# Optimization experiments

Hardware: AMD Instinct MI355X
Metric: run time of the kernel (lower is better)

Reference implementation:

```python
import math
import jax, jax.numpy as jnp
import numpy as np


def setup_inputs() -> dict:
    key = jax.random.key(0)
    kq, kk, kv = jax.random.split(key, 3)
    bs, n_tok, n_heads, width = 2, 2048, 8, 64
    deg = 32  # neighbors per dst token -> coo_cnt_max
    q = jax.random.normal(kq, (bs, n_tok, n_heads, width), dtype=jnp.float32)
    k = jax.random.normal(kk, (bs, n_tok, n_heads, width), dtype=jnp.float32)
    v = jax.random.normal(kv, (bs, n_tok, n_heads, width), dtype=jnp.float32)
    rng = np.random.default_rng(0)
    dst = np.repeat(np.arange(n_tok), deg)            # [cl]
    src = rng.integers(0, n_tok, size=n_tok * deg)    # [cl]
    sm = np.tile(np.arange(deg), n_tok)               # [cl], unique per dst
    coo = jnp.asarray(np.stack([dst, src, sm], axis=1), dtype=jnp.int32)  # [cl,3]
    return {"q": q, "k": k, "v": v, "coo": coo, "coo_cnt_max": deg}


def reference(q, k, v, coo, coo_cnt_max):
    bs, n_tok, n_heads, width = q.shape
    dst, src, sm = coo[:, 0], coo[:, 1], coo[:, 2]
    # [b, h, t, w] layout
    qq = q.transpose(0, 2, 1, 3)
    kk = k.transpose(0, 2, 1, 3)
    vv = v.transpose(0, 2, 1, 3)
    scale = -1.0 / math.sqrt(width)
    # per-edge negative scaled L1 distance: [b, h, cl]
    ww = jnp.sum(jnp.abs(qq[:, :, dst, :] - kk[:, :, src, :]), axis=-1) * scale
    neg_big = jnp.asarray(-1e32, dtype=q.dtype)
    # scatter edge scores into dense padded attention slots: [b, h, t, cnt+1]
    attn = jnp.full((bs, n_heads, n_tok, coo_cnt_max + 1), neg_big, dtype=q.dtype)
    attn = attn.at[:, :, dst, sm].set(ww)
    attn_sm = jax.nn.softmax(attn, axis=-1)
    # scatter values into padded neighbor-value tensor: [b, h, t, cnt+1, w]
    vw = jnp.zeros((bs, n_heads, n_tok, coo_cnt_max + 1, width), dtype=q.dtype)
    vw = vw.at[:, :, dst, sm, :].set(vv[:, :, src, :])
    vo = jnp.einsum('bhds,bhdsw->bdhw', attn_sm, vw)
    # only dst tokens appearing in coo receive output; others stay zero
    vout = jnp.zeros_like(v).at[:, dst, :, :].set(vo[:, dst, :, :])
    return vout
```

## Files before the change

### kernel.cpp

```cpp
#include <hip/hip_runtime.h>
#include <hip/hip_bf16.h>

#define BS   2
#define NT   2048
#define NH   8
#define WD   64
#define DEG  32

#define PK_ROWS   (BS * 4 * NT)
#define PK_ROW_B  512
#define PK_UINTS  (PK_ROWS * (PK_ROW_B / 4))

typedef _Float16 half2_t __attribute__((ext_vector_type(2)));

#if defined(__has_builtin)
#if __has_builtin(__builtin_amdgcn_fdot2)
#define HAVE_FDOT2 1
#endif
#endif

__device__ __forceinline__ unsigned short f2h(float f) {
    _Float16 h = (_Float16)f;
    unsigned short u; __builtin_memcpy(&u, &h, 2); return u;
}
__device__ __forceinline__ half2_t u2h2(unsigned int w) {
    half2_t r; __builtin_memcpy(&r, &w, 4); return r;
}
__device__ __forceinline__ half2_t habs2(half2_t x) {
    unsigned int u; __builtin_memcpy(&u, &x, 4);
    u &= 0x7fff7fffu;
    half2_t r; __builtin_memcpy(&r, &u, 4); return r;
}

__global__ __launch_bounds__(256) void pack_kv_f16(
    const float* __restrict__ k,
    const float* __restrict__ v,
    unsigned int* __restrict__ packed)
{
    const int u    = blockIdx.x * 256 + threadIdx.x;
    const int row  = u >> 7;
    const int pos  = u & 127;
    const int part = pos >> 6;
    const int e    = pos & 63;
    const int s    = row & (NT - 1);
    const int hp   = (row >> 11) & 3;
    const int b    = row >> 13;
    const int elem = e * 2;
    const int h_in = elem >> 6;
    const int w0   = elem & 63;

    const float* src = (part == 0 ? k : v)
        + (((size_t)(b * NT + s) * NH + hp * 2 + h_in) << 6) + w0;
    float2 f = *(const float2*)src;
    packed[u] = (unsigned int)f2h(f.x) | ((unsigned int)f2h(f.y) << 16);
}

__global__ __launch_bounds__(64) void l1attn_main_f16(
    const float* __restrict__ q,
    const unsigned int* __restrict__ packed,
    const int* __restrict__ coo,
    float* __restrict__ out)
{
    const int bid   = blockIdx.x;
    const int combo = bid & 7;
    const int hp    = combo & 3;
    const int b     = combo >> 2;
    const int t     = bid >> 3;
    const int ln    = threadIdx.x;
    const int hw    = ln >> 5;
    const int l     = ln & 31;

    __shared__ int          s_src[DEG];
    __shared__ unsigned int s_q[64];
    __shared__ unsigned int s_k[DEG * 128];

    if (ln < DEG) {
        s_src[ln] = coo[(t * DEG + ln) * 3 + 1];
    }
    {
        const float2* qrow = (const float2*)
            (q + ((size_t)(b * NT + t) * NH + hp * 2) * WD);
        float2 qv = qrow[ln];
        s_q[ln] = (unsigned int)f2h(qv.x) | ((unsigned int)f2h(qv.y) << 16);
    }
    __syncthreads();

    {
        #pragma unroll
        for (int r = 0; r < 16; ++r) {
            const int j = 2 * r + hw;
            const int s = s_src[j];
            const int chunk = (l + j) & 31;
            const char* gaddr = (const char*)packed
                + ((size_t)((b * 4 + hp) * NT + s)) * PK_ROW_B + chunk * 16;
            char* laddr = (char*)s_k + 2 * r * PK_ROW_B;
            __builtin_amdgcn_global_load_lds(
                (const __attribute__((address_space(1))) void*)gaddr,
                (__attribute__((address_space(3))) void*)laddr,
                16, 0, 0);
        }
    }
    __syncthreads();

    float acc = 0.f;
#ifdef HAVE_FDOT2
    const half2_t one2 = {(_Float16)1.0f, (_Float16)1.0f};
#endif
    #pragma unroll
    for (int i = 0; i < 8; ++i) {
        const int slot = ((hw * 8 + i) - l) & 31;
        uint4 c = *(const uint4*)((const char*)s_k + l * PK_ROW_B + slot * 16);
        const unsigned int ws[4] = {c.x, c.y, c.z, c.w};
        #pragma unroll
        for (int m = 0; m < 4; ++m) {
            half2_t kh = u2h2(ws[m]);
            half2_t qh = u2h2(s_q[hw * 32 + i * 4 + m]);
            half2_t ad = habs2(qh - kh);
#ifdef HAVE_FDOT2
            acc = __builtin_amdgcn_fdot2(ad, one2, acc, false);
#else
            acc += (float)ad.x + (float)ad.y;
#endif
        }
    }
    float logit = -0.125f * acc;

    float m = logit;
    #pragma unroll
    for (int d = 16; d >= 1; d >>= 1) m = fmaxf(m, __shfl_xor(m, d));
    float e = __expf(logit - m);
    float ssum = e;
    #pragma unroll
    for (int d = 16; d >= 1; d >>= 1) ssum += __shfl_xor(ssum, d);
    const float p = e / ssum;

    int p2i;
    {
        _Float16 ph = (_Float16)p;
        half2_t p2 = {ph, ph};
        __builtin_memcpy(&p2i, &p2, 4);
    }
    const int gv   = 16 + hw * 8 + (l >> 2);
    const int boff = (l & 3) * 4;
    half2_t acc2 = {(_Float16)0.0f, (_Float16)0.0f};
    #pragma unroll 8
    for (int j = 0; j < DEG; ++j) {
        const int pj2i = __shfl(p2i, j, 32);
        const int slot = (gv - j) & 31;
        unsigned int w = *(const unsigned int*)
            ((const char*)s_k + j * PK_ROW_B + slot * 16 + boff);
        acc2 = __builtin_elementwise_fma(u2h2(pj2i), u2h2(w), acc2);
    }

    const int h = hp * 2 + hw;
    float2 res = make_float2((float)acc2.x, (float)acc2.y);
    *(float2*)(out + ((size_t)(b * NT + t) * NH + h) * WD + 2 * l) = res;
}

__global__ __launch_bounds__(64) void l1attn_sparse_fp32(
    const float* __restrict__ q,
    const float* __restrict__ k,
    const float* __restrict__ v,
    const int* __restrict__ coo,
    float* __restrict__ out)
{
    const int bid   = blockIdx.x;
    const int combo = bid & 7;
    const int hp    = combo & 3;
    const int b     = combo >> 2;
    const int t     = bid >> 3;
    const int ln    = threadIdx.x;
    const int hw    = ln >> 5;
    const int l     = ln & 31;

    __shared__ int   s_src[DEG];
    __shared__ float s_q[2 * WD];
    __shared__ float s_k[DEG * 2 * WD];

    if (ln < DEG) s_src[ln] = coo[(t * DEG + ln) * 3 + 1];
    {
        const float2* qrow = (const float2*)
            (q + ((size_t)(b * NT + t) * NH + hp * 2) * WD);
        float2 qv = qrow[ln];
        s_q[2 * ln] = qv.x; s_q[2 * ln + 1] = qv.y;
    }
    __syncthreads();
    {
        #pragma unroll
        for (int r = 0; r < 16; ++r) {
            const int j = 2 * r + hw;
            const int s = s_src[j];
            const int chunk = (l + j) & 31;
            const float* gaddr = k + ((size_t)(b * NT + s) * NH + hp * 2) * WD
                               + chunk * 4;
            float* laddr = s_k + 2 * r * (2 * WD);
            __builtin_amdgcn_global_load_lds(
                (const __attribute__((address_space(1))) void*)gaddr,
                (__attribute__((address_space(3))) void*)laddr, 16, 0, 0);
        }
    }
    const int h  = hp * 2 + hw;
    const int jg = l >> 4;
    const int wq = l & 15;
    float4 vr[16];
    #pragma unroll
    for (int i = 0; i < 16; ++i) {
        const int sv = s_src[2 * i + jg];
        vr[i] = *(const float4*)(v + ((size_t)(b * NT + sv) * NH + h) * WD + 4 * wq);
    }
    __syncthreads();
    const float* qh = s_q + hw * WD;
    float acc = 0.f;
    #pragma unroll
    for (int i = 0; i < 16; ++i) {
        const int slot = ((hw * 16 + i) - l) & 31;
        float4 kv = *(const float4*)(s_k + l * (2 * WD) + slot * 4);
        const int wb = i * 4;
        acc += fabsf(qh[wb] - kv.x) + fabsf(qh[wb + 1] - kv.y)
             + fabsf(qh[wb + 2] - kv.z) + fabsf(qh[wb + 3] - kv.w);
    }
    float logit = -0.125f * acc;
    float m = logit;
    #pragma unroll
    for (int d = 16; d >= 1; d >>= 1) m = fmaxf(m, __shfl_xor(m, d));
    float e = __expf(logit - m);
    float ssum = e;
    #pragma unroll
    for (int d = 16; d >= 1; d >>= 1) ssum += __shfl_xor(ssum, d);
    const float p = e / ssum;
    float4 o4 = make_float4(0.f, 0.f, 0.f, 0.f);
    #pragma unroll
    for (int i = 0; i < 16; ++i) {
        const float pj = __shfl(p, 2 * i + jg, 32);
        o4.x += pj * vr[i].x; o4.y += pj * vr[i].y;
        o4.z += pj * vr[i].z; o4.w += pj * vr[i].w;
    }
    o4.x += __shfl_xor(o4.x, 16); o4.y += __shfl_xor(o4.y, 16);
    o4.z += __shfl_xor(o4.z, 16); o4.w += __shfl_xor(o4.w, 16);
    if (jg == 0)
        *(float4*)(out + ((size_t)(b * NT + t) * NH + h) * WD + 4 * wq) = o4;
}

extern "C" void kernel_launch(void* const* d_in, const int* in_sizes, int n_in,
                              void* d_out, int out_size, void* d_ws, size_t ws_size,
                              hipStream_t stream) {
    const float* q   = (const float*)d_in[0];
    const float* k   = (const float*)d_in[1];
    const float* v   = (const float*)d_in[2];
    const int*   coo = (const int*)d_in[3];
    float*       o   = (float*)d_out;

    if (ws_size >= (size_t)PK_UINTS * 4) {
        unsigned int* packed = (unsigned int*)d_ws;
        hipLaunchKernelGGL(pack_kv_f16, dim3(PK_UINTS / 256), dim3(256), 0,
                           stream, k, v, packed);
        hipLaunchKernelGGL(l1attn_main_f16, dim3(BS * NT * 4), dim3(64), 0,
                           stream, q, packed, coo, o);
    } else {
        hipLaunchKernelGGL(l1attn_sparse_fp32, dim3(BS * NT * 4), dim3(64), 0,
                           stream, q, k, v, coo, o);
    }
}
```

Measured before the change: 108.8 us.

## Process several tokens per block with double-buffered async LDS prefetch

Each 64-thread block now handles 8 destination tokens instead of one, so the grid shrinks by 8x. The coo source indices and the q rows for all 8 tokens are loaded up front. The gathered K/V rows for the next token are prefetched into a second LDS buffer with global_load_lds while the current token is computed. Manual vmcnt waits replace the block barriers. This is meant to hide gather latency and amortise per-block setup, but it cuts the number of resident waves and doubles LDS per block, which may reduce latency hiding across the GPU.

Measured after the change: 114.7 us. 1.05x slower.

```diff
diff --git a/kernel.cpp b/kernel.cpp
--- a/kernel.cpp
+++ b/kernel.cpp
@@ -6,6 +6,7 @@
 #define NH   8
 #define WD   64
 #define DEG  32
+#define TPB  8
 
 #define PK_ROWS   (BS * 4 * NT)
 #define PK_ROW_B  512
@@ -65,96 +66,114 @@
     const int combo = bid & 7;
     const int hp    = combo & 3;
     const int b     = combo >> 2;
-    const int t     = bid >> 3;
+    const int tbase = (bid >> 3) * TPB;
     const int ln    = threadIdx.x;
     const int hw    = ln >> 5;
     const int l     = ln & 31;
 
-    __shared__ int          s_src[DEG];
-    __shared__ unsigned int s_q[64];
-    __shared__ unsigned int s_k[DEG * 128];
-
-    if (ln < DEG) {
-        s_src[ln] = coo[(t * DEG + ln) * 3 + 1];
-    }
-    {
+    __shared__ int          s_src[TPB * DEG];
+    __shared__ unsigned int s_q[TPB * 64];
+    __shared__ unsigned int s_buf[2][DEG * 128];
+
+    #pragma unroll
+    for (int x = 0; x < (TPB * DEG) / 64; ++x) {
+        const int idx = x * 64 + ln;
+        const int tt  = idx >> 5, j = idx & 31;
+        s_src[idx] = coo[((tbase + tt) * DEG + j) * 3 + 1];
+    }
+    #pragma unroll
+    for (int tt = 0; tt < TPB; ++tt) {
         const float2* qrow = (const float2*)
-            (q + ((size_t)(b * NT + t) * NH + hp * 2) * WD);
+            (q + ((size_t)(b * NT + tbase + tt) * NH + hp * 2) * WD);
         float2 qv = qrow[ln];
-        s_q[ln] = (unsigned int)f2h(qv.x) | ((unsigned int)f2h(qv.y) << 16);
-    }
-    __syncthreads();
-
-    {
+        s_q[tt * 64 + ln] = (unsigned int)f2h(qv.x)
+                          | ((unsigned int)f2h(qv.y) << 16);
+    }
+    asm volatile("s_waitcnt vmcnt(0)" ::: "memory");
+
+    auto issue = [&](int pb, int tt) {
         #pragma unroll
         for (int r = 0; r < 16; ++r) {
             const int j = 2 * r + hw;
-            const int s = s_src[j];
+            const int s = s_src[tt * DEG + j];
             const int chunk = (l + j) & 31;
             const char* gaddr = (const char*)packed
                 + ((size_t)((b * 4 + hp) * NT + s)) * PK_ROW_B + chunk * 16;
-            char* laddr = (char*)s_k + 2 * r * PK_ROW_B;
+            char* laddr = (char*)&s_buf[pb][0] + 2 * r * PK_ROW_B;
             __builtin_amdgcn_global_load_lds(
                 (const __attribute__((address_space(1))) void*)gaddr,
                 (__attribute__((address_space(3))) void*)laddr,
                 16, 0, 0);
         }
-    }
-    __syncthreads();
-
-    float acc = 0.f;
+    };
+
+    issue(0, 0);
+
+    #pragma unroll
+    for (int it = 0; it < TPB; ++it) {
+        if (it + 1 < TPB) issue((it + 1) & 1, it + 1);
+
+        if (it == 0)            asm volatile("s_waitcnt vmcnt(16)" ::: "memory");
+        else if (it == TPB - 1) asm volatile("s_waitcnt vmcnt(1)"  ::: "memory");
+        else                    asm volatile("s_waitcnt vmcnt(17)" ::: "memory");
+
+        const unsigned int* buf = &s_buf[it & 1][0];
+
+        float acc = 0.f;
 #ifdef HAVE_FDOT2
-    const half2_t one2 = {(_Float16)1.0f, (_Float16)1.0f};
-#endif
-    #pragma unroll
-    for (int i = 0; i < 8; ++i) {
-        const int slot = ((hw * 8 + i) - l) & 31;
-        uint4 c = *(const uint4*)((const char*)s_k + l * PK_ROW_B + slot * 16);
-        const unsigned int ws[4] = {c.x, c.y, c.z, c.w};
-        #pragma unroll
-        for (int m = 0; m < 4; ++m) {
-            half2_t kh = u2h2(ws[m]);
-            half2_t qh = u2h2(s_q[hw * 32 + i * 4 + m]);
-            half2_t ad = habs2(qh - kh);
+        const half2_t one2 = {(_Float16)1.0f, (_Float16)1.0f};
+#endif
+        #pragma unroll
+        for (int i = 0; i < 8; ++i) {
+            const int slot = ((hw * 8 + i) - l) & 31;
+            uint4 c = *(const uint4*)((const char*)buf + l * PK_ROW_B + slot * 16);
+            const unsigned int ws[4] = {c.x, c.y, c.z, c.w};
+            #pragma unroll
+            for (int m = 0; m < 4; ++m) {
+                half2_t kh = u2h2(ws[m]);
+                half2_t qh = u2h2(s_q[it * 64 + hw * 32 + i * 4 + m]);
+                half2_t ad = habs2(qh - kh);
 #ifdef HAVE_FDOT2
-            acc = __builtin_amdgcn_fdot2(ad, one2, acc, false);
+                acc = __builtin_amdgcn_fdot2(ad, one2, acc, false);
 #else
-            acc += (float)ad.x + (float)ad.y;
-#endif
-        }
-    }
-    float logit = -0.125f * acc;
-
-    float m = logit;
-    #pragma unroll
-    for (int d = 16; d >= 1; d >>= 1) m = fmaxf(m, __shfl_xor(m, d));
-    float e = __expf(logit - m);
-    float ssum = e;
-    #pragma unroll
-    for (int d = 16; d >= 1; d >>= 1) ssum += __shfl_xor(ssum, d);
-    const float p = e / ssum;
-
-    int p2i;
-    {
-        _Float16 ph = (_Float16)p;
-        half2_t p2 = {ph, ph};
-        __builtin_memcpy(&p2i, &p2, 4);
-    }
-    const int gv   = 16 + hw * 8 + (l >> 2);
-    const int boff = (l & 3) * 4;
-    half2_t acc2 = {(_Float16)0.0f, (_Float16)0.0f};
-    #pragma unroll 8
-    for (int j = 0; j < DEG; ++j) {
-        const int pj2i = __shfl(p2i, j, 32);
-        const int slot = (gv - j) & 31;
-        unsigned int w = *(const unsigned int*)
-            ((const char*)s_k + j * PK_ROW_B + slot * 16 + boff);
-        acc2 = __builtin_elementwise_fma(u2h2(pj2i), u2h2(w), acc2);
-    }
-
-    const int h = hp * 2 + hw;
-    float2 res = make_float2((float)acc2.x, (float)acc2.y);
-    *(float2*)(out + ((size_t)(b * NT + t) * NH + h) * WD + 2 * l) = res;
+                acc += (float)ad.x + (float)ad.y;
+#endif
+            }
+        }
+        float logit = -0.125f * acc;
+
+        float m = logit;
+        #pragma unroll
+        for (int d = 16; d >= 1; d >>= 1) m = fmaxf(m, __shfl_xor(m, d));
+        float e = __expf(logit - m);
+        float ssum = e;
+        #pragma unroll
+        for (int d = 16; d >= 1; d >>= 1) ssum += __shfl_xor(ssum, d);
+        const float p = e / ssum;
+
+        int p2i;
+        {
+            _Float16 ph = (_Float16)p;
+            half2_t p2 = {ph, ph};
+            __builtin_memcpy(&p2i, &p2, 4);
+        }
+        const int gv   = 16 + hw * 8 + (l >> 2);
+        const int boff = (l & 3) * 4;
+        half2_t acc2 = {(_Float16)0.0f, (_Float16)0.0f};
+        #pragma unroll 8
+        for (int j = 0; j < DEG; ++j) {
+            const int pj2i = __shfl(p2i, j, 32);
+            const int slot = (gv - j) & 31;
+            unsigned int w = *(const unsigned int*)
+                ((const char*)buf + j * PK_ROW_B + slot * 16 + boff);
+            acc2 = __builtin_elementwise_fma(u2h2(pj2i), u2h2(w), acc2);
+        }
+
+        const int h = hp * 2 + hw;
+        const int t = tbase + it;
+        float2 res = make_float2((float)acc2.x, (float)acc2.y);
+        *(float2*)(out + ((size_t)(b * NT + t) * NH + h) * WD + 2 * l) = res;
+    }
 }
 
 __global__ __launch_bounds__(64) void l1attn_sparse_fp32(
@@ -254,8 +273,8 @@
         unsigned int* packed = (unsigned int*)d_ws;
         hipLaunchKernelGGL(pack_kv_f16, dim3(PK_UINTS / 256), dim3(256), 0,
                            stream, k, v, packed);
-        hipLaunchKernelGGL(l1attn_main_f16, dim3(BS * NT * 4), dim3(64), 0,
-                           stream, q, packed, coo, o);
+        hipLaunchKernelGGL(l1attn_main_f16, dim3((BS * NT * 4) / TPB), dim3(64),
+                           0, stream, q, packed, coo, o);
     } else {
         hipLaunchKernelGGL(l1attn_sparse_fp32, dim3(BS * NT * 4), dim3(64), 0,
                            stream, q, k, v, coo, o);
```

## Stage only K to LDS and load V into registers, overlapping with L1 compute

Applied to the files above, without the earlier changes.

The f16 main kernel now copies only the K half of each packed neighbor row into LDS, which halves shared memory per block. V is loaded straight into registers with per-lane 8-byte loads. A partial vmcnt wait replaces the barrier, so the L1 distance computation can start while the V loads are still in flight. The weighted V sum becomes a register FMA across half-wave groups followed by a cross-lane xor reduction. The s_waitcnt vmcnt(16) count is a hand-tuned inline assembly wait, and removing the __syncthreads means LDS data written by other lanes is read without a barrier, which may be unsafe.

New measurement: 98.01 us. -9.9%, faster.

```diff
diff --git a/kernel.cpp b/kernel.cpp
--- a/kernel.cpp
+++ b/kernel.cpp
@@ -26,10 +26,12 @@
 __device__ __forceinline__ half2_t u2h2(unsigned int w) {
     half2_t r; __builtin_memcpy(&r, &w, 4); return r;
 }
+__device__ __forceinline__ unsigned int h22u(half2_t h) {
+    unsigned int u; __builtin_memcpy(&u, &h, 4); return u;
+}
 __device__ __forceinline__ half2_t habs2(half2_t x) {
-    unsigned int u; __builtin_memcpy(&u, &x, 4);
-    u &= 0x7fff7fffu;
-    half2_t r; __builtin_memcpy(&r, &u, 4); return r;
+    unsigned int u = h22u(x) & 0x7fff7fffu;
+    return u2h2(u);
 }
 
 __global__ __launch_bounds__(256) void pack_kv_f16(
@@ -72,7 +74,7 @@
 
     __shared__ int          s_src[DEG];
     __shared__ unsigned int s_q[64];
-    __shared__ unsigned int s_k[DEG * 128];
+    __shared__ unsigned int s_k[DEG * 64];
 
     if (ln < DEG) {
         s_src[ln] = coo[(t * DEG + ln) * 3 + 1];
@@ -85,22 +87,40 @@
     }
     __syncthreads();
 
-    {
-        #pragma unroll
-        for (int r = 0; r < 16; ++r) {
-            const int j = 2 * r + hw;
+    const size_t combo_base = (size_t)((b * 4 + hp) * NT) * (PK_ROW_B / 4);
+
+    {
+        const int rsub = ln >> 4;
+        const int c    = ln & 15;
+        #pragma unroll
+        for (int r = 0; r < 8; ++r) {
+            const int j = 4 * r + rsub;
             const int s = s_src[j];
-            const int chunk = (l + j) & 31;
-            const char* gaddr = (const char*)packed
-                + ((size_t)((b * 4 + hp) * NT + s)) * PK_ROW_B + chunk * 16;
-            char* laddr = (char*)s_k + 2 * r * PK_ROW_B;
+            const int chunk = (c + j) & 15;
+            const char* gaddr = (const char*)(packed + combo_base)
+                              + (size_t)s * PK_ROW_B + chunk * 16;
+            char* laddr = (char*)s_k + 4 * r * 256;
             __builtin_amdgcn_global_load_lds(
                 (const __attribute__((address_space(1))) void*)gaddr,
                 (__attribute__((address_space(3))) void*)laddr,
                 16, 0, 0);
         }
     }
-    __syncthreads();
+
+    const int jg = l >> 4;
+    const int wq = l & 15;
+    uint2 vr[16];
+    {
+        const char* vbase = (const char*)(packed + combo_base)
+                          + (16 + hw * 8) * 16 + wq * 8;
+        #pragma unroll
+        for (int i = 0; i < 16; ++i) {
+            const int sv = s_src[2 * i + jg];
+            vr[i] = *(const uint2*)(vbase + (size_t)sv * PK_ROW_B);
+        }
+    }
+
+    asm volatile("s_waitcnt vmcnt(16)" ::: "memory");
 
     float acc = 0.f;
 #ifdef HAVE_FDOT2
@@ -108,8 +128,8 @@
 #endif
     #pragma unroll
     for (int i = 0; i < 8; ++i) {
-        const int slot = ((hw * 8 + i) - l) & 31;
-        uint4 c = *(const uint4*)((const char*)s_k + l * PK_ROW_B + slot * 16);
+        const int slot = ((hw * 8 + i) - l) & 15;
+        uint4 c = *(const uint4*)((const char*)s_k + l * 256 + slot * 16);
         const unsigned int ws[4] = {c.x, c.y, c.z, c.w};
         #pragma unroll
         for (int m = 0; m < 4; ++m) {
@@ -138,23 +158,31 @@
     {
         _Float16 ph = (_Float16)p;
         half2_t p2 = {ph, ph};
-        __builtin_memcpy(&p2i, &p2, 4);
-    }
-    const int gv   = 16 + hw * 8 + (l >> 2);
-    const int boff = (l & 3) * 4;
-    half2_t acc2 = {(_Float16)0.0f, (_Float16)0.0f};
-    #pragma unroll 8
-    for (int j = 0; j < DEG; ++j) {
-        const int pj2i = __shfl(p2i, j, 32);
-        const int slot = (gv - j) & 31;
-        unsigned int w = *(const unsigned int*)
-            ((const char*)s_k + j * PK_ROW_B + slot * 16 + boff);
-        acc2 = __builtin_elementwise_fma(u2h2(pj2i), u2h2(w), acc2);
-    }
-
-    const int h = hp * 2 + hw;
-    float2 res = make_float2((float)acc2.x, (float)acc2.y);
-    *(float2*)(out + ((size_t)(b * NT + t) * NH + h) * WD + 2 * l) = res;
+        p2i = h22u(p2);
+    }
+    half2_t a0 = {(_Float16)0.0f, (_Float16)0.0f};
+    half2_t a1 = a0;
+    #pragma unroll
+    for (int i = 0; i < 16; ++i) {
+        const int pj2i = __shfl(p2i, 2 * i + jg, 32);
+        half2_t pj2 = u2h2(pj2i);
+        a0 = __builtin_elementwise_fma(pj2, u2h2(vr[i].x), a0);
+        a1 = __builtin_elementwise_fma(pj2, u2h2(vr[i].y), a1);
+    }
+    {
+        unsigned int u0 = h22u(a0), u1 = h22u(a1);
+        unsigned int o0 = __shfl_xor((int)u0, 16);
+        unsigned int o1 = __shfl_xor((int)u1, 16);
+        a0 = a0 + u2h2(o0);
+        a1 = a1 + u2h2(o1);
+    }
+
+    if (jg == 0) {
+        const int h = hp * 2 + hw;
+        float4 res = make_float4((float)a0.x, (float)a0.y,
+                                 (float)a1.x, (float)a1.y);
+        *(float4*)(out + ((size_t)(b * NT + t) * NH + h) * WD + 4 * wq) = res;
+    }
 }
 
 __global__ __launch_bounds__(64) void l1attn_sparse_fp32(
```
